# Kernel optimization log

Measured on AMD Instinct MI355X. Metric: run time of the kernel, lower is better.

Reference implementation:

```python
import jax, jax.numpy as jnp
import numpy as np

BQ, BK = 128, 64  # SpargeAttn-style Q/K block sizes
NEG = -1e30


def _block_mask(q, k, simthreshd1, cdfthreshd, scale):
    """Mean-similarity block selection: a (q-block, k-block) pair is pruned only
    when both blocks are self-similar (mean cosine sim to block mean exceeds the
    per-head simthreshd1) AND it is not in the top-CDF mass (cdfthreshd) of the
    compressed block-level softmax."""
    B, H, L, D = q.shape
    nq, nk = L // BQ, L // BK
    qb = q.reshape(B, H, nq, BQ, D)
    kb = k.reshape(B, H, nk, BK, D)
    qm = qb.mean(3)  # [B,H,nq,D] block means
    km = kb.mean(3)  # [B,H,nk,D]

    def blocksim(xb, xm):
        xn = xb / (jnp.linalg.norm(xb, axis=-1, keepdims=True) + 1e-6)
        mn = xm / (jnp.linalg.norm(xm, axis=-1, keepdims=True) + 1e-6)
        return jnp.einsum('bhntd,bhnd->bhnt', xn, mn).mean(-1)  # [B,H,n]

    th = simthreshd1[None, :, None]
    comp_q = blocksim(qb, qm) > th  # [B,H,nq] self-similar q blocks
    comp_k = blocksim(kb, km) > th  # [B,H,nk]

    # compressed attention over block means, then CDF-based top-mass selection
    p = jax.nn.softmax(jnp.einsum('bhqd,bhkd->bhqk', qm, km) * scale, axis=-1)
    order = jnp.argsort(-p, axis=-1)
    sp = jnp.take_along_axis(p, order, axis=-1)
    csum = jnp.cumsum(sp, axis=-1)
    keep_sorted = (csum - sp) < cdfthreshd[None, :, None, None]  # prefix covering tau
    rank = jnp.argsort(order, axis=-1)  # inverse permutation
    selected = jnp.take_along_axis(keep_sorted, rank, axis=-1)  # [B,H,nq,nk]

    return selected | ~(comp_q[..., :, None] & comp_k[..., None, :])


def setup_inputs() -> dict:
    key = jax.random.key(0)
    kq, kk, kv, kc = jax.random.split(key, 4)
    B, H, L, D = 1, 16, 2048, 64
    return {
        'q': jax.random.normal(kq, (B, H, L, D), dtype=jnp.float32),
        'k': jax.random.normal(kk, (B, H, L, D), dtype=jnp.float32),
        'v': jax.random.normal(kv, (B, H, L, D), dtype=jnp.float32),
        'simthreshd1': jnp.zeros((H,), dtype=jnp.float32),
        'cdfthreshd': jax.random.uniform(kc, (H,), dtype=jnp.float32),
    }


def reference(q, k, v, simthreshd1, cdfthreshd):
    B, H, L, D = q.shape
    scale = 1.0 / np.sqrt(D).astype(np.float32)
    # smooth_k: subtract per-(B,H) key mean (softmax-invariant shift, matches kernel)
    k = k - k.mean(axis=-2, keepdims=True)
    bmask = _block_mask(q, k, simthreshd1, cdfthreshd, scale)  # [B,H,nq,nk] bool
    mask_tok = jnp.repeat(jnp.repeat(bmask, BQ, axis=2), BK, axis=3)  # [B,H,L,L]
    s = jnp.einsum('bhqd,bhkd->bhqk', q, k) * scale
    s = jnp.where(mask_tok, s, NEG)
    p = jax.nn.softmax(s, axis=-1)
    return jnp.einsum('bhqk,bhkd->bhqd', p, v)
```

## Files before the change

### kernel.cpp

```cpp
#include <hip/hip_runtime.h>

#define HH 16
#define LL 2048
#define DD 64
#define BQ 128
#define BK 64
#define NQ (LL/BQ)
#define NK (LL/BK)
#define SCALE 0.125f
#define QSCALE (0.125f * 1.44269504f)

typedef __attribute__((ext_vector_type(8))) short s8v;
typedef __attribute__((ext_vector_type(4))) float f4v;

static __device__ __forceinline__ ushort f2bf(float x) {
    unsigned u = __float_as_uint(x);
    u += 0x7fff + ((u >> 16) & 1);
    return (ushort)(u >> 16);
}

#define GLOAD(src, dst) \
    __builtin_amdgcn_global_load_lds((const __attribute__((address_space(1))) unsigned int*)(src), \
                                     (__attribute__((address_space(3))) unsigned int*)(dst), 16, 0, 0)

#define VMWAIT4 do { asm volatile("s_waitcnt vmcnt(4)" ::: "memory"); __builtin_amdgcn_sched_barrier(0); } while(0)
#define VMWAIT0 do { asm volatile("s_waitcnt vmcnt(0)" ::: "memory"); __builtin_amdgcn_sched_barrier(0); } while(0)
#define BARRIER do { __builtin_amdgcn_s_barrier(); __builtin_amdgcn_sched_barrier(0); } while(0)

__global__ void kmean1_kernel(const float* __restrict__ k, float* __restrict__ kpart) {
    int b = blockIdx.x;
    int h = blockIdx.y;
    int t = threadIdx.x;
    int d = t & 63, c = t >> 6;
    const float* kh = k + ((size_t)h*LL + (size_t)b*256) * DD;
    float s = 0.f;
    for (int l = c*64; l < c*64 + 64; ++l) s += kh[(size_t)l * DD + d];
    __shared__ float red[4][64];
    red[c][d] = s;
    __syncthreads();
    if (t < 64) kpart[((size_t)h*8 + b)*64 + t] = red[0][t]+red[1][t]+red[2][t]+red[3][t];
}

__global__ __launch_bounds__(128) void stats_kernel(
        const float* __restrict__ q, const float* __restrict__ k, const float* __restrict__ v,
        const float* __restrict__ kpart, const float* __restrict__ simth,
        float* __restrict__ qm, float* __restrict__ km,
        int* __restrict__ compq, int* __restrict__ compk,
        ushort* __restrict__ qb, ushort* __restrict__ kb, ushort* __restrict__ vTb) {
    __shared__ __align__(16) char smem[34304];
    int h = blockIdx.y, t = threadIdx.x;

    if ((int)blockIdx.x < NQ) {
        int qi = blockIdx.x;
        float (*xs)[DD+1] = (float(*)[DD+1])smem;
        float* mean = (float*)(smem + 33280);
        float* red  = (float*)(smem + 33536);
        size_t row = (size_t)h*LL + (size_t)qi*BQ + t;
        const float* rp = q + row * DD;
        float x[DD]; float n2 = 0.f;
        #pragma unroll
        for (int d = 0; d < DD; d += 4) {
            float4 v4 = *(const float4*)(rp + d);
            x[d]=v4.x; x[d+1]=v4.y; x[d+2]=v4.z; x[d+3]=v4.w;
            n2 += v4.x*v4.x + v4.y*v4.y + v4.z*v4.z + v4.w*v4.w;
        }
        #pragma unroll
        for (int d = 0; d < DD; d += 4) {
            ushort4 o;
            o.x = f2bf(x[d]*QSCALE);   o.y = f2bf(x[d+1]*QSCALE);
            o.z = f2bf(x[d+2]*QSCALE); o.w = f2bf(x[d+3]*QSCALE);
            *(ushort4*)(qb + row*DD + d) = o;
        }
        #pragma unroll
        for (int d = 0; d < DD; ++d) xs[t][d] = x[d];
        __syncthreads();
        if (t < DD) {
            float s = 0.f;
            for (int r = 0; r < BQ; ++r) s += xs[r][t];
            mean[t] = s * (1.0f/BQ);
        }
        __syncthreads();
        float dot = 0.f, m2 = 0.f;
        #pragma unroll
        for (int d = 0; d < DD; ++d) { dot += x[d]*mean[d]; m2 += mean[d]*mean[d]; }
        float cs = dot / ((sqrtf(n2) + 1e-6f) * (sqrtf(m2) + 1e-6f));
        red[t] = cs; __syncthreads();
        for (int sft = BQ/2; sft > 0; sft >>= 1) {
            if (t < sft) red[t] += red[t + sft];
            __syncthreads();
        }
        if (t == 0) compq[h*NQ + qi] = (red[0] * (1.0f/BQ)) > simth[h] ? 1 : 0;
        if (t < DD) qm[((size_t)h*NQ + qi)*DD + t] = mean[t];
    } else {
        int ki = blockIdx.x - NQ;
        float* mu_s = (float*)smem;
        float (*xs)[DD+1] = (float(*)[DD+1])(smem + 256);
        ushort (*vs)[66]  = (ushort(*)[66])(smem + 256 + 16640);
        float* mean = (float*)(smem + 256 + 16640 + 8448);
        float* red  = (float*)(smem + 256 + 16640 + 8448 + 256);
        if (t < 64) {
            float s = 0.f;
            #pragma unroll
            for (int b = 0; b < 8; ++b) s += kpart[((size_t)h*8 + b)*64 + t];
            mu_s[t] = s * (1.0f/LL);
        }
        __syncthreads();
        size_t rowb = (size_t)h*LL + (size_t)ki*BK;
        float x[DD]; float n2 = 0.f;
        if (t < 64) {
            const float* rp = k + (rowb + t) * DD;
            #pragma unroll
            for (int d = 0; d < DD; d += 4) {
                float4 v4 = *(const float4*)(rp + d);
                v4.x -= mu_s[d]; v4.y -= mu_s[d+1]; v4.z -= mu_s[d+2]; v4.w -= mu_s[d+3];
                x[d]=v4.x; x[d+1]=v4.y; x[d+2]=v4.z; x[d+3]=v4.w;
                n2 += v4.x*v4.x + v4.y*v4.y + v4.z*v4.z + v4.w*v4.w;
            }
            #pragma unroll
            for (int d = 0; d < DD; d += 4) {
                ushort4 o;
                o.x = f2bf(x[d]);   o.y = f2bf(x[d+1]);
                o.z = f2bf(x[d+2]); o.w = f2bf(x[d+3]);
                *(ushort4*)(kb + (rowb + t)*DD + d) = o;
            }
            #pragma unroll
            for (int d = 0; d < DD; ++d) xs[t][d] = x[d];
        } else {
            int tk = t - 64;
            const float* vp = v + (rowb + tk) * DD;
            #pragma unroll
            for (int d = 0; d < DD; d += 4) {
                float4 v4 = *(const float4*)(vp + d);
                vs[tk][d]   = f2bf(v4.x); vs[tk][d+1] = f2bf(v4.y);
                vs[tk][d+2] = f2bf(v4.z); vs[tk][d+3] = f2bf(v4.w);
            }
        }
        __syncthreads();
        if (t < 64) {
            size_t vbase = ((size_t)h*DD + t)*LL + (size_t)ki*64;
            #pragma unroll
            for (int r8 = 0; r8 < 64; r8 += 8) {
                s8v o;
                #pragma unroll
                for (int e = 0; e < 8; ++e) o[e] = (short)vs[r8+e][t];
                *(s8v*)(vTb + vbase + r8) = o;
            }
            float s = 0.f;
            for (int r = 0; r < BK; ++r) s += xs[r][t];
            mean[t] = s * (1.0f/BK);
        }
        __syncthreads();
        if (t < 64) {
            float dot = 0.f, m2 = 0.f;
            #pragma unroll
            for (int d = 0; d < DD; ++d) { dot += x[d]*mean[d]; m2 += mean[d]*mean[d]; }
            float cs = dot / ((sqrtf(n2) + 1e-6f) * (sqrtf(m2) + 1e-6f));
            red[t] = cs;
        }
        __syncthreads();
        for (int sft = 32; sft > 0; sft >>= 1) {
            if (t < sft) red[t] += red[t + sft];
            __syncthreads();
        }
        if (t == 0) compk[h*NK + ki] = (red[0] * (1.0f/BK)) > simth[h] ? 1 : 0;
        if (t < 64) km[((size_t)h*NK + ki)*DD + t] = mean[t];
    }
}

__global__ __launch_bounds__(256, 2) void attn_kernel(
        const ushort* __restrict__ qb, const ushort* __restrict__ kb,
        const ushort* __restrict__ vTb,
        const float* __restrict__ qm, const float* __restrict__ km,
        const int* __restrict__ compq, const int* __restrict__ compk,
        const float* __restrict__ cdfth, float* __restrict__ out) {
    __shared__ __align__(16) ushort ldsK[3][64*64];
    __shared__ __align__(16) ushort ldsV[3][64*64];
    __shared__ __align__(16) ushort plds[4][16][72];
    __shared__ unsigned mskS;

    int h    = blockIdx.y;
    int qi   = blockIdx.x >> 1;
    int half = blockIdx.x & 1;
    int tid  = threadIdx.x;
    int w    = tid >> 6;
    int l    = tid & 63;
    int lo = l & 15, hi = l >> 4;
    int r0 = qi*BQ + half*64 + w*16;

    const ushort* qh = qb  + (size_t)h*LL*DD;
    const char*   kh = (const char*)(kb  + (size_t)h*LL*DD);
    const char*   vh = (const char*)(vTb + (size_t)h*DD*LL);

    s8v qa[2];
    #pragma unroll
    for (int kk = 0; kk < 2; ++kk)
        qa[kk] = *(const s8v*)(qh + (size_t)(r0 + lo)*DD + kk*32 + hi*8);

    if (tid < 64) {
        int j = l & 31;
        const float* qv = qm + ((size_t)h*NQ + qi)*DD;
        const float* kv = km + ((size_t)h*NK + j)*DD;
        float s = 0.f;
        for (int d = 0; d < DD; ++d) s += qv[d]*kv[d];
        s *= SCALE;
        float m = s;
        #pragma unroll
        for (int xm = 1; xm <= 16; xm <<= 1) m = fmaxf(m, __shfl_xor(m, xm, 32));
        float e = expf(s - m);
        float den = 0.f;
        for (int i = 0; i < 32; ++i) den += __shfl(e, i, 32);
        float p = e / den;
        float mass = 0.f;
        for (int i = 0; i < 32; ++i) {
            float pi = __shfl(p, i, 32);
            if (pi > p || (pi == p && i < j)) mass += pi;
        }
        int keep = (mass < cdfth[h]) || !(compq[h*NQ+qi] && compk[h*NK+j]);
        unsigned long long bal = __ballot(keep != 0);
        if (l == 0) mskS = (unsigned)bal;
    }
    __syncthreads();
    unsigned msk = mskS;

    int srow = l >> 3;
    int sgx  = ((l & 7) ^ srow) * 16;
    int c0 = 2*w, c1 = 2*w + 1;
    size_t ks0 = (size_t)(c0*8 + srow)*128 + sgx;
    size_t ks1 = (size_t)(c1*8 + srow)*128 + sgx;
    size_t vs0 = (size_t)(c0*8 + srow)*(LL*2) + sgx;
    size_t vs1 = (size_t)(c1*8 + srow)*(LL*2) + sgx;
    int dst0 = c0*1024, dst1 = c1*1024;

    int p0 = (hi)     ^ (lo & 7);
    int p1 = (4 + hi) ^ (lo & 7);
    int kidx0 = lo*64 + p0*8;
    int kidx1 = lo*64 + p1*8;

    f4v O[4];
    float mrun = -1e30f, lrun = 0.f;
    #pragma unroll
    for (int nd = 0; nd < 4; ++nd) O[nd] = (f4v){0.f, 0.f, 0.f, 0.f};

    auto stage = [&](int buf, int j) {
        const char* kj = kh + (size_t)j*8192;
        const char* vj = vh + (size_t)j*128;
        char* kd = (char*)&ldsK[buf][0];
        char* vd = (char*)&ldsV[buf][0];
        GLOAD(kj + ks0, kd + dst0);
        GLOAD(kj + ks1, kd + dst1);
        GLOAD(vj + vs0, vd + dst0);
        GLOAD(vj + vs1, vd + dst1);
    };

    auto compute = [&](const ushort* Kb, const ushort* Vb) {
        f4v S[4];
        #pragma unroll
        for (int ni = 0; ni < 4; ++ni) S[ni] = (f4v){0.f, 0.f, 0.f, 0.f};
        __builtin_amdgcn_s_setprio(1);
        #pragma unroll
        for (int ni = 0; ni < 4; ++ni) {
            s8v kf0 = *(const s8v*)(Kb + ni*1024 + kidx0);
            s8v kf1 = *(const s8v*)(Kb + ni*1024 + kidx1);
            S[ni] = __builtin_amdgcn_mfma_f32_16x16x32_bf16(kf0, qa[0], S[ni], 0, 0, 0);
            S[ni] = __builtin_amdgcn_mfma_f32_16x16x32_bf16(kf1, qa[1], S[ni], 0, 0, 0);
        }
        __builtin_amdgcn_s_setprio(0);
        float pm;
        {
            float a0 = fmaxf(fmaxf(S[0][0],S[0][1]), fmaxf(S[0][2],S[0][3]));
            float a1 = fmaxf(fmaxf(S[1][0],S[1][1]), fmaxf(S[1][2],S[1][3]));
            float a2 = fmaxf(fmaxf(S[2][0],S[2][1]), fmaxf(S[2][2],S[2][3]));
            float a3 = fmaxf(fmaxf(S[3][0],S[3][1]), fmaxf(S[3][2],S[3][3]));
            pm = fmaxf(fmaxf(a0,a1), fmaxf(a2,a3));
        }
        pm = fmaxf(pm, __shfl_xor(pm, 16));
        pm = fmaxf(pm, __shfl_xor(pm, 32));
        if (__any(pm > mrun + 8.0f)) {
            float mnew = fmaxf(mrun, pm);
            float alpha = __builtin_amdgcn_exp2f(mrun - mnew);
            lrun *= alpha;
            #pragma unroll
            for (int r = 0; r < 4; ++r) {
                float a = __shfl(alpha, hi*4 + r);
                #pragma unroll
                for (int nd = 0; nd < 4; ++nd) O[nd][r] *= a;
            }
            mrun = mnew;
        }
        f4v P4[4];
        float ps = 0.f;
        #pragma unroll
        for (int ni = 0; ni < 4; ++ni)
            #pragma unroll
            for (int r = 0; r < 4; ++r) {
                float p = __builtin_amdgcn_exp2f(S[ni][r] - mrun);
                P4[ni][r] = p;
                ps += p;
            }
        lrun += ps;
        #pragma unroll
        for (int ni = 0; ni < 4; ++ni) {
            unsigned c01, c23;
            asm("v_cvt_pk_bf16_f32 %0, %1, %2" : "=v"(c01) : "v"(P4[ni][0]), "v"(P4[ni][1]));
            asm("v_cvt_pk_bf16_f32 %0, %1, %2" : "=v"(c23) : "v"(P4[ni][2]), "v"(P4[ni][3]));
            *(uint2*)&plds[w][lo][ni*16 + hi*4] = make_uint2(c01, c23);
        }
        __builtin_amdgcn_s_setprio(1);
        #pragma unroll
        for (int kk = 0; kk < 2; ++kk) {
            s8v pa = *(const s8v*)&plds[w][lo][kk*32 + hi*8];
            int kidx = kk ? kidx1 : kidx0;
            #pragma unroll
            for (int nd = 0; nd < 4; ++nd) {
                s8v vf = *(const s8v*)(Vb + nd*1024 + kidx);
                O[nd] = __builtin_amdgcn_mfma_f32_16x16x32_bf16(pa, vf, O[nd], 0, 0, 0);
            }
        }
        __builtin_amdgcn_s_setprio(0);
    };

    int ja = __ffs(msk) - 1; msk &= msk - 1;
    stage(0, ja);
    int jb = msk ? __ffs(msk) - 1 : -1; msk &= msk - 1;
    if (jb >= 0) stage(1, jb);
    int jc;
    for (;;) {
        if (jb >= 0) { VMWAIT4; } else { VMWAIT0; }
        BARRIER;
        jc = msk ? __ffs(msk) - 1 : -1; msk &= msk - 1;
        if (jc >= 0) stage(2, jc);
        compute(&ldsK[0][0], &ldsV[0][0]);
        if (jb < 0) break;
        if (jc >= 0) { VMWAIT4; } else { VMWAIT0; }
        BARRIER;
        ja = msk ? __ffs(msk) - 1 : -1; msk &= msk - 1;
        if (ja >= 0) stage(0, ja);
        compute(&ldsK[1][0], &ldsV[1][0]);
        if (jc < 0) break;
        if (ja >= 0) { VMWAIT4; } else { VMWAIT0; }
        BARRIER;
        jb = msk ? __ffs(msk) - 1 : -1; msk &= msk - 1;
        if (jb >= 0) stage(1, jb);
        compute(&ldsK[2][0], &ldsV[2][0]);
        if (ja < 0) break;
    }

    float ltot = lrun;
    ltot += __shfl_xor(ltot, 16);
    ltot += __shfl_xor(ltot, 32);
    #pragma unroll
    for (int r = 0; r < 4; ++r) {
        float lr = __shfl(ltot, hi*4 + r);
        float inv = 1.0f / lr;
        int row = r0 + hi*4 + r;
        float* orow = out + ((size_t)h*LL + row)*DD;
        #pragma unroll
        for (int nd = 0; nd < 4; ++nd)
            orow[nd*16 + lo] = O[nd][r] * inv;
    }
}

extern "C" void kernel_launch(void* const* d_in, const int* in_sizes, int n_in,
                              void* d_out, int out_size, void* d_ws, size_t ws_size,
                              hipStream_t stream) {
    const float* q     = (const float*)d_in[0];
    const float* k     = (const float*)d_in[1];
    const float* v     = (const float*)d_in[2];
    const float* simth = (const float*)d_in[3];
    const float* cdfth = (const float*)d_in[4];
    float* out = (float*)d_out;

    float* ws    = (float*)d_ws;
    float* kpart = ws;
    float* qm    = kpart + HH*8*64;
    float* km    = qm + HH*NQ*DD;
    int*   compq = (int*)(km + HH*NK*DD);
    int*   compk = compq + HH*NQ;
    size_t off = (size_t)((char*)(compk + HH*NK) - (char*)d_ws);
    off = (off + 15) & ~(size_t)15;
    ushort* qbuf = (ushort*)((char*)d_ws + off);
    ushort* kbuf = qbuf + (size_t)HH*LL*DD;
    ushort* vTb  = kbuf + (size_t)HH*LL*DD;

    kmean1_kernel<<<dim3(8, HH), 256, 0, stream>>>(k, kpart);
    stats_kernel<<<dim3(NQ + NK, HH), 128, 0, stream>>>(q, k, v, kpart, simth,
                                                        qm, km, compq, compk,
                                                        qbuf, kbuf, vTb);
    attn_kernel<<<dim3(NQ*2, HH), 256, 0, stream>>>(qbuf, kbuf, vTb,
                                                    qm, km, compq, compk, cdfth, out);
}
```

Measured before the change: 78.23 us.

## Split KV blocks across warps with register-resident tiles and LDS merge

Reworks the attention kernel so each of the four warps handles all 64 query rows of the block but only a strided subset of the selected K/V blocks, loading K and V fragments straight from global memory into registers instead of staging them through LDS with async copies and barriers. Partial softmax states (m, l, O) from each warp are merged through shared memory at the end. The block-mask computation moves into its own small kernel that writes a bitmask. This removes the per-iteration barriers and the LDS staging, at the cost of many more registers per thread (O[4][4], S[4][4]), about 68 KB of LDS, an extra kernel launch, and uncoalesced, unpipelined global loads.

```diff
diff --git a/kernel.cpp b/kernel.cpp
--- a/kernel.cpp
+++ b/kernel.cpp
@@ -18,14 +18,6 @@
     u += 0x7fff + ((u >> 16) & 1);
     return (ushort)(u >> 16);
 }
-
-#define GLOAD(src, dst) \
-    __builtin_amdgcn_global_load_lds((const __attribute__((address_space(1))) unsigned int*)(src), \
-                                     (__attribute__((address_space(3))) unsigned int*)(dst), 16, 0, 0)
-
-#define VMWAIT4 do { asm volatile("s_waitcnt vmcnt(4)" ::: "memory"); __builtin_amdgcn_sched_barrier(0); } while(0)
-#define VMWAIT0 do { asm volatile("s_waitcnt vmcnt(0)" ::: "memory"); __builtin_amdgcn_sched_barrier(0); } while(0)
-#define BARRIER do { __builtin_amdgcn_s_barrier(); __builtin_amdgcn_sched_barrier(0); } while(0)
 
 __global__ void kmean1_kernel(const float* __restrict__ k, float* __restrict__ kpart) {
     int b = blockIdx.x;
@@ -167,16 +159,46 @@
     }
 }
 
+__global__ void bmask_kernel(const float* __restrict__ qm, const float* __restrict__ km,
+                             const int* __restrict__ compq, const int* __restrict__ compk,
+                             const float* __restrict__ cdfth, unsigned* __restrict__ bmaskbits) {
+    int qi = blockIdx.x, h = blockIdx.y;
+    int j = threadIdx.x;
+    __shared__ float ssh[NK];
+    __shared__ float p[NK];
+    const float* qv = qm + ((size_t)h*NQ + qi)*DD;
+    const float* kv = km + ((size_t)h*NK + j)*DD;
+    float s = 0.f;
+    for (int d = 0; d < DD; ++d) s += qv[d]*kv[d];
+    ssh[j] = s * SCALE;
+    __syncthreads();
+    float m = ssh[0];
+    for (int i = 1; i < NK; ++i) m = fmaxf(m, ssh[i]);
+    float den = 0.f;
+    for (int i = 0; i < NK; ++i) den += expf(ssh[i] - m);
+    p[j] = expf(ssh[j] - m) / den;
+    __syncthreads();
+    float pj = p[j];
+    float mass = 0.f;
+    for (int i = 0; i < NK; ++i) {
+        float pi = p[i];
+        if (pi > pj || (pi == pj && i < j)) mass += pi;
+    }
+    int sel = (mass < cdfth[h]) ? 1 : 0;
+    int keep = (sel || !(compq[h*NQ+qi] && compk[h*NK+j])) ? 1 : 0;
+    unsigned long long bal = __ballot(keep);
+    if (j == 0) bmaskbits[h*NQ + qi] = (unsigned)bal;
+}
+
 __global__ __launch_bounds__(256, 2) void attn_kernel(
         const ushort* __restrict__ qb, const ushort* __restrict__ kb,
-        const ushort* __restrict__ vTb,
-        const float* __restrict__ qm, const float* __restrict__ km,
-        const int* __restrict__ compq, const int* __restrict__ compk,
-        const float* __restrict__ cdfth, float* __restrict__ out) {
-    __shared__ __align__(16) ushort ldsK[3][64*64];
-    __shared__ __align__(16) ushort ldsV[3][64*64];
-    __shared__ __align__(16) ushort plds[4][16][72];
-    __shared__ unsigned mskS;
+        const ushort* __restrict__ vTb, const unsigned* __restrict__ bmaskbits,
+        float* __restrict__ out) {
+    __shared__ __align__(16) char shmem[69632];
+    ushort* pl = (ushort*)(shmem) + (threadIdx.x >> 6) * 64 * 80;
+    float*  Ob = (float*)shmem;
+    float*  mb = (float*)(shmem + 67584);
+    float*  lb = (float*)(shmem + 68608);
 
     int h    = blockIdx.y;
     int qi   = blockIdx.x >> 1;
@@ -185,178 +207,177 @@
     int w    = tid >> 6;
     int l    = tid & 63;
     int lo = l & 15, hi = l >> 4;
-    int r0 = qi*BQ + half*64 + w*16;
+    int r0 = qi*BQ + half*64;
+
+    unsigned msk = bmaskbits[h*NQ + qi];
 
     const ushort* qh = qb  + (size_t)h*LL*DD;
-    const char*   kh = (const char*)(kb  + (size_t)h*LL*DD);
-    const char*   vh = (const char*)(vTb + (size_t)h*DD*LL);
-
-    s8v qa[2];
+    const ushort* kh = kb  + (size_t)h*LL*DD;
+    const ushort* vh = vTb + (size_t)h*DD*LL;
+
+    s8v qf[4][2];
     #pragma unroll
-    for (int kk = 0; kk < 2; ++kk)
-        qa[kk] = *(const s8v*)(qh + (size_t)(r0 + lo)*DD + kk*32 + hi*8);
-
-    if (tid < 64) {
-        int j = l & 31;
-        const float* qv = qm + ((size_t)h*NQ + qi)*DD;
-        const float* kv = km + ((size_t)h*NK + j)*DD;
-        float s = 0.f;
-        for (int d = 0; d < DD; ++d) s += qv[d]*kv[d];
-        s *= SCALE;
-        float m = s;
-        #pragma unroll
-        for (int xm = 1; xm <= 16; xm <<= 1) m = fmaxf(m, __shfl_xor(m, xm, 32));
-        float e = expf(s - m);
-        float den = 0.f;
-        for (int i = 0; i < 32; ++i) den += __shfl(e, i, 32);
-        float p = e / den;
-        float mass = 0.f;
-        for (int i = 0; i < 32; ++i) {
-            float pi = __shfl(p, i, 32);
-            if (pi > p || (pi == p && i < j)) mass += pi;
-        }
-        int keep = (mass < cdfth[h]) || !(compq[h*NQ+qi] && compk[h*NK+j]);
-        unsigned long long bal = __ballot(keep != 0);
-        if (l == 0) mskS = (unsigned)bal;
-    }
+    for (int qt = 0; qt < 4; ++qt)
+        #pragma unroll
+        for (int kk = 0; kk < 2; ++kk)
+            qf[qt][kk] = *(const s8v*)(qh + (size_t)(r0 + qt*16 + lo)*DD + kk*32 + hi*8);
+
+    f4v O[4][4];
+    float m[4], lsum[4];
+    #pragma unroll
+    for (int qt = 0; qt < 4; ++qt) {
+        m[qt] = -1e30f; lsum[qt] = 0.f;
+        #pragma unroll
+        for (int dt = 0; dt < 4; ++dt) O[qt][dt] = (f4v){0.f,0.f,0.f,0.f};
+    }
+
+    unsigned mm = msk; int rank = 0;
+    while (mm) {
+        int j = __ffs(mm) - 1; mm &= mm - 1;
+        if (((rank++) & 3) != w) continue;
+
+        const ushort* kbj = kh + (size_t)j*BK*DD;
+        const ushort* vbj = vh + (size_t)j*BK;
+
+        s8v kf[4][2];
+        #pragma unroll
+        for (int kt = 0; kt < 4; ++kt)
+            #pragma unroll
+            for (int kk = 0; kk < 2; ++kk)
+                kf[kt][kk] = *(const s8v*)(kbj + (size_t)(kt*16 + lo)*DD + kk*32 + hi*8);
+
+        f4v S[4][4];
+        #pragma unroll
+        for (int kt = 0; kt < 4; ++kt)
+            #pragma unroll
+            for (int qt = 0; qt < 4; ++qt)
+                S[kt][qt] = (f4v){0.f,0.f,0.f,0.f};
+        __builtin_amdgcn_s_setprio(1);
+        #pragma unroll
+        for (int kk = 0; kk < 2; ++kk)
+            #pragma unroll
+            for (int kt = 0; kt < 4; ++kt)
+                #pragma unroll
+                for (int qt = 0; qt < 4; ++qt)
+                    S[kt][qt] = __builtin_amdgcn_mfma_f32_16x16x32_bf16(kf[kt][kk], qf[qt][kk], S[kt][qt], 0, 0, 0);
+        __builtin_amdgcn_s_setprio(0);
+
+        s8v vf[2][4];
+        #pragma unroll
+        for (int kk = 0; kk < 2; ++kk)
+            #pragma unroll
+            for (int dt = 0; dt < 4; ++dt)
+                vf[kk][dt] = *(const s8v*)(vbj + (size_t)(dt*16 + lo)*LL + kk*32 + hi*8);
+
+        float pm[4];
+        #pragma unroll
+        for (int qt = 0; qt < 4; ++qt) {
+            float a0 = fmaxf(fmaxf(S[0][qt][0],S[0][qt][1]), fmaxf(S[0][qt][2],S[0][qt][3]));
+            float a1 = fmaxf(fmaxf(S[1][qt][0],S[1][qt][1]), fmaxf(S[1][qt][2],S[1][qt][3]));
+            float a2 = fmaxf(fmaxf(S[2][qt][0],S[2][qt][1]), fmaxf(S[2][qt][2],S[2][qt][3]));
+            float a3 = fmaxf(fmaxf(S[3][qt][0],S[3][qt][1]), fmaxf(S[3][qt][2],S[3][qt][3]));
+            float p = fmaxf(fmaxf(a0,a1), fmaxf(a2,a3));
+            p = fmaxf(p, __shfl_xor(p, 16));
+            p = fmaxf(p, __shfl_xor(p, 32));
+            pm[qt] = p;
+        }
+        bool grow = (pm[0] > m[0]+8.0f) | (pm[1] > m[1]+8.0f) |
+                    (pm[2] > m[2]+8.0f) | (pm[3] > m[3]+8.0f);
+        if (__any(grow)) {
+            float alpha[4];
+            #pragma unroll
+            for (int qt = 0; qt < 4; ++qt) {
+                float mn = fmaxf(m[qt], pm[qt]);
+                alpha[qt] = __builtin_amdgcn_exp2f(m[qt] - mn);
+                lsum[qt] *= alpha[qt];
+                m[qt] = mn;
+            }
+            #pragma unroll
+            for (int qt = 0; qt < 4; ++qt)
+                #pragma unroll
+                for (int r = 0; r < 4; ++r) {
+                    float a = __shfl(alpha[qt], hi*4 + r);
+                    #pragma unroll
+                    for (int dt = 0; dt < 4; ++dt) O[qt][dt][r] *= a;
+                }
+        }
+        #pragma unroll
+        for (int qt = 0; qt < 4; ++qt) {
+            float ps = 0.f;
+            #pragma unroll
+            for (int kt = 0; kt < 4; ++kt) {
+                float p0 = __builtin_amdgcn_exp2f(S[kt][qt][0] - m[qt]);
+                float p1 = __builtin_amdgcn_exp2f(S[kt][qt][1] - m[qt]);
+                float p2 = __builtin_amdgcn_exp2f(S[kt][qt][2] - m[qt]);
+                float p3 = __builtin_amdgcn_exp2f(S[kt][qt][3] - m[qt]);
+                ps += (p0 + p1) + (p2 + p3);
+                unsigned c01, c23;
+                asm("v_cvt_pk_bf16_f32 %0, %1, %2" : "=v"(c01) : "v"(p0), "v"(p1));
+                asm("v_cvt_pk_bf16_f32 %0, %1, %2" : "=v"(c23) : "v"(p2), "v"(p3));
+                *(uint2*)&pl[(qt*16 + lo)*80 + kt*16 + hi*4] = make_uint2(c01, c23);
+            }
+            lsum[qt] += ps;
+        }
+        __builtin_amdgcn_s_setprio(1);
+        #pragma unroll
+        for (int qt = 0; qt < 4; ++qt)
+            #pragma unroll
+            for (int kk = 0; kk < 2; ++kk) {
+                s8v pa = *(const s8v*)&pl[(qt*16 + lo)*80 + kk*32 + hi*8];
+                #pragma unroll
+                for (int dt = 0; dt < 4; ++dt)
+                    O[qt][dt] = __builtin_amdgcn_mfma_f32_16x16x32_bf16(pa, vf[kk][dt], O[qt][dt], 0, 0, 0);
+            }
+        __builtin_amdgcn_s_setprio(0);
+    }
+
+    #pragma unroll
+    for (int qt = 0; qt < 4; ++qt) {
+        lsum[qt] += __shfl_xor(lsum[qt], 16);
+        lsum[qt] += __shfl_xor(lsum[qt], 32);
+    }
+
     __syncthreads();
-    unsigned msk = mskS;
-
-    int srow = l >> 3;
-    int sgx  = ((l & 7) ^ srow) * 16;
-    int c0 = 2*w, c1 = 2*w + 1;
-    size_t ks0 = (size_t)(c0*8 + srow)*128 + sgx;
-    size_t ks1 = (size_t)(c1*8 + srow)*128 + sgx;
-    size_t vs0 = (size_t)(c0*8 + srow)*(LL*2) + sgx;
-    size_t vs1 = (size_t)(c1*8 + srow)*(LL*2) + sgx;
-    int dst0 = c0*1024, dst1 = c1*1024;
-
-    int p0 = (hi)     ^ (lo & 7);
-    int p1 = (4 + hi) ^ (lo & 7);
-    int kidx0 = lo*64 + p0*8;
-    int kidx1 = lo*64 + p1*8;
-
-    f4v O[4];
-    float mrun = -1e30f, lrun = 0.f;
+
+    if (hi == 0) {
+        #pragma unroll
+        for (int qt = 0; qt < 4; ++qt) {
+            mb[w*64 + qt*16 + lo] = m[qt];
+            lb[w*64 + qt*16 + lo] = lsum[qt];
+        }
+    }
     #pragma unroll
-    for (int nd = 0; nd < 4; ++nd) O[nd] = (f4v){0.f, 0.f, 0.f, 0.f};
-
-    auto stage = [&](int buf, int j) {
-        const char* kj = kh + (size_t)j*8192;
-        const char* vj = vh + (size_t)j*128;
-        char* kd = (char*)&ldsK[buf][0];
-        char* vd = (char*)&ldsV[buf][0];
-        GLOAD(kj + ks0, kd + dst0);
-        GLOAD(kj + ks1, kd + dst1);
-        GLOAD(vj + vs0, vd + dst0);
-        GLOAD(vj + vs1, vd + dst1);
-    };
-
-    auto compute = [&](const ushort* Kb, const ushort* Vb) {
-        f4v S[4];
-        #pragma unroll
-        for (int ni = 0; ni < 4; ++ni) S[ni] = (f4v){0.f, 0.f, 0.f, 0.f};
-        __builtin_amdgcn_s_setprio(1);
-        #pragma unroll
-        for (int ni = 0; ni < 4; ++ni) {
-            s8v kf0 = *(const s8v*)(Kb + ni*1024 + kidx0);
-            s8v kf1 = *(const s8v*)(Kb + ni*1024 + kidx1);
-            S[ni] = __builtin_amdgcn_mfma_f32_16x16x32_bf16(kf0, qa[0], S[ni], 0, 0, 0);
-            S[ni] = __builtin_amdgcn_mfma_f32_16x16x32_bf16(kf1, qa[1], S[ni], 0, 0, 0);
-        }
-        __builtin_amdgcn_s_setprio(0);
-        float pm;
-        {
-            float a0 = fmaxf(fmaxf(S[0][0],S[0][1]), fmaxf(S[0][2],S[0][3]));
-            float a1 = fmaxf(fmaxf(S[1][0],S[1][1]), fmaxf(S[1][2],S[1][3]));
-            float a2 = fmaxf(fmaxf(S[2][0],S[2][1]), fmaxf(S[2][2],S[2][3]));
-            float a3 = fmaxf(fmaxf(S[3][0],S[3][1]), fmaxf(S[3][2],S[3][3]));
-            pm = fmaxf(fmaxf(a0,a1), fmaxf(a2,a3));
-        }
-        pm = fmaxf(pm, __shfl_xor(pm, 16));
-        pm = fmaxf(pm, __shfl_xor(pm, 32));
-        if (__any(pm > mrun + 8.0f)) {
-            float mnew = fmaxf(mrun, pm);
-            float alpha = __builtin_amdgcn_exp2f(mrun - mnew);
-            lrun *= alpha;
-            #pragma unroll
-            for (int r = 0; r < 4; ++r) {
-                float a = __shfl(alpha, hi*4 + r);
-                #pragma unroll
-                for (int nd = 0; nd < 4; ++nd) O[nd][r] *= a;
-            }
-            mrun = mnew;
-        }
-        f4v P4[4];
-        float ps = 0.f;
-        #pragma unroll
-        for (int ni = 0; ni < 4; ++ni)
-            #pragma unroll
-            for (int r = 0; r < 4; ++r) {
-                float p = __builtin_amdgcn_exp2f(S[ni][r] - mrun);
-                P4[ni][r] = p;
-                ps += p;
-            }
-        lrun += ps;
-        #pragma unroll
-        for (int ni = 0; ni < 4; ++ni) {
-            unsigned c01, c23;
-            asm("v_cvt_pk_bf16_f32 %0, %1, %2" : "=v"(c01) : "v"(P4[ni][0]), "v"(P4[ni][1]));
-            asm("v_cvt_pk_bf16_f32 %0, %1, %2" : "=v"(c23) : "v"(P4[ni][2]), "v"(P4[ni][3]));
-            *(uint2*)&plds[w][lo][ni*16 + hi*4] = make_uint2(c01, c23);
-        }
-        __builtin_amdgcn_s_setprio(1);
-        #pragma unroll
-        for (int kk = 0; kk < 2; ++kk) {
-            s8v pa = *(const s8v*)&plds[w][lo][kk*32 + hi*8];
-            int kidx = kk ? kidx1 : kidx0;
-            #pragma unroll
-            for (int nd = 0; nd < 4; ++nd) {
-                s8v vf = *(const s8v*)(Vb + nd*1024 + kidx);
-                O[nd] = __builtin_amdgcn_mfma_f32_16x16x32_bf16(pa, vf, O[nd], 0, 0, 0);
-            }
-        }
-        __builtin_amdgcn_s_setprio(0);
-    };
-
-    int ja = __ffs(msk) - 1; msk &= msk - 1;
-    stage(0, ja);
-    int jb = msk ? __ffs(msk) - 1 : -1; msk &= msk - 1;
-    if (jb >= 0) stage(1, jb);
-    int jc;
-    for (;;) {
-        if (jb >= 0) { VMWAIT4; } else { VMWAIT0; }
-        BARRIER;
-        jc = msk ? __ffs(msk) - 1 : -1; msk &= msk - 1;
-        if (jc >= 0) stage(2, jc);
-        compute(&ldsK[0][0], &ldsV[0][0]);
-        if (jb < 0) break;
-        if (jc >= 0) { VMWAIT4; } else { VMWAIT0; }
-        BARRIER;
-        ja = msk ? __ffs(msk) - 1 : -1; msk &= msk - 1;
-        if (ja >= 0) stage(0, ja);
-        compute(&ldsK[1][0], &ldsV[1][0]);
-        if (jc < 0) break;
-        if (ja >= 0) { VMWAIT4; } else { VMWAIT0; }
-        BARRIER;
-        jb = msk ? __ffs(msk) - 1 : -1; msk &= msk - 1;
-        if (jb >= 0) stage(1, jb);
-        compute(&ldsK[2][0], &ldsV[2][0]);
-        if (ja < 0) break;
-    }
-
-    float ltot = lrun;
-    ltot += __shfl_xor(ltot, 16);
-    ltot += __shfl_xor(ltot, 32);
-    #pragma unroll
-    for (int r = 0; r < 4; ++r) {
-        float lr = __shfl(ltot, hi*4 + r);
-        float inv = 1.0f / lr;
-        int row = r0 + hi*4 + r;
-        float* orow = out + ((size_t)h*LL + row)*DD;
-        #pragma unroll
-        for (int nd = 0; nd < 4; ++nd)
-            orow[nd*16 + lo] = O[nd][r] * inv;
+    for (int qt = 0; qt < 4; ++qt)
+        #pragma unroll
+        for (int dt = 0; dt < 4; ++dt)
+            #pragma unroll
+            for (int r = 0; r < 4; ++r)
+                Ob[w*4224 + (qt*16 + hi*4 + r)*66 + dt*16 + lo] = O[qt][dt][r];
+    __syncthreads();
+
+    {
+        int q = l;
+        float mw0 = mb[q], mw1 = mb[64+q], mw2 = mb[128+q], mw3 = mb[192+q];
+        float ms = fmaxf(fmaxf(mw0,mw1), fmaxf(mw2,mw3));
+        float c0 = __builtin_amdgcn_exp2f(mw0 - ms);
+        float c1 = __builtin_amdgcn_exp2f(mw1 - ms);
+        float c2 = __builtin_amdgcn_exp2f(mw2 - ms);
+        float c3 = __builtin_amdgcn_exp2f(mw3 - ms);
+        float ls = lb[q]*c0 + lb[64+q]*c1 + lb[128+q]*c2 + lb[192+q]*c3;
+        float inv = 1.0f / ls;
+        float* orow = out + ((size_t)h*LL + r0 + q)*DD + w*16;
+        #pragma unroll
+        for (int i4 = 0; i4 < 4; ++i4) {
+            float4 o;
+            #pragma unroll
+            for (int e = 0; e < 4; ++e) {
+                int d = w*16 + i4*4 + e;
+                float acc = Ob[q*66 + d]*c0 + Ob[4224 + q*66 + d]*c1
+                          + Ob[8448 + q*66 + d]*c2 + Ob[12672 + q*66 + d]*c3;
+                ((float*)&o)[e] = acc * inv;
+            }
+            *(float4*)(orow + i4*4) = o;
+        }
     }
 }
 
@@ -376,7 +397,8 @@
     float* km    = qm + HH*NQ*DD;
     int*   compq = (int*)(km + HH*NK*DD);
     int*   compk = compq + HH*NQ;
-    size_t off = (size_t)((char*)(compk + HH*NK) - (char*)d_ws);
+    unsigned* bmb = (unsigned*)(compk + HH*NK);
+    size_t off = (size_t)((char*)(bmb + HH*NQ) - (char*)d_ws);
     off = (off + 15) & ~(size_t)15;
     ushort* qbuf = (ushort*)((char*)d_ws + off);
     ushort* kbuf = qbuf + (size_t)HH*LL*DD;
@@ -386,6 +408,6 @@
     stats_kernel<<<dim3(NQ + NK, HH), 128, 0, stream>>>(q, k, v, kpart, simth,
                                                         qm, km, compq, compk,
                                                         qbuf, kbuf, vTb);
-    attn_kernel<<<dim3(NQ*2, HH), 256, 0, stream>>>(qbuf, kbuf, vTb,
-                                                    qm, km, compq, compk, cdfth, out);
-}
+    bmask_kernel<<<dim3(NQ, HH), NK, 0, stream>>>(qm, km, compq, compk, cdfth, bmb);
+    attn_kernel<<<dim3(NQ*2, HH), 256, 0, stream>>>(qbuf, kbuf, vTb, bmb, out);
+}
```

Result: faster. 75.28 us (-3.8%).
